# Optimization experiments

Hardware: AMD Instinct MI355X
Metric: run time of the kernel (lower is better)

Reference implementation:

```python
import jax, jax.numpy as jnp
import numpy as np

B, S, D, H, DK, DV = 4, 2048, 512, 8, 64, 64


def setup_inputs() -> dict:
    key0 = jax.random.key(0)
    ks = jax.random.split(key0, 11)
    w = 0.02
    return {
        "query": jax.random.normal(ks[0], (B, S, D), dtype=jnp.float32),
        "key": jax.random.normal(ks[1], (B, S, D), dtype=jnp.float32),
        "value": jax.random.normal(ks[2], (B, S, D), dtype=jnp.float32),
        "Wq": jax.random.normal(ks[3], (D, DK), dtype=jnp.float32) * w,
        "bq": jnp.zeros((DK,), dtype=jnp.float32),
        "Wk": jax.random.normal(ks[4], (D, DK), dtype=jnp.float32) * w,
        "bk": jnp.zeros((DK,), dtype=jnp.float32),
        "Wv": jax.random.normal(ks[5], (D, DV), dtype=jnp.float32) * w,
        "bv": jnp.zeros((DV,), dtype=jnp.float32),
        "Wo": jax.random.normal(ks[6], (H * DV, D), dtype=jnp.float32) * w,
        "bo": jnp.zeros((D,), dtype=jnp.float32),
    }


def reference(query, key, value, Wq, bq, Wk, bk, Wv, bv, Wo, bo):
    # NOTE: original module applies the SAME Dense layers to every head
    # (q_list = [self.query(query) for _ in range(heads)]), so all H heads
    # are mathematically identical -> compute one head and replicate.
    # NOTE: V is projected from `key`, not `value` (faithful to source bug).
    q = query @ Wq + bq          # [B, S, DK]
    k = key @ Wk + bk            # [B, S, DK]
    v = key @ Wv + bv            # [B, S, DV]
    scale = np.sqrt(DK).astype(np.float32)
    scores = jnp.einsum("bqd,bkd->bqk", q, k) / scale  # [B, S, S]
    # masked_mha=True and training=True -> causal mask, fill -1e19
    causal = jnp.triu(jnp.ones((S, S), dtype=scores.dtype), 1)
    scores = scores + causal * jnp.asarray(-1e19, scores.dtype)
    attn = jax.nn.softmax(scores, axis=-1)              # [B, S, S]
    o = jnp.einsum("bqk,bkv->bqv", attn, v)             # [B, S, DV]
    # concat of H identical heads along last axis == tile
    concat = jnp.tile(o, (1, 1, H))                     # [B, S, H*DV]
    return concat @ Wo + bo                             # [B, S, D]
```

## Files before the change

kernel.cpp:

```cpp
#include <hip/hip_runtime.h>
#include <hip/hip_bf16.h>


#define BB 4
#define SS 2048
#define BS (BB*SS)
#define MSHIFT 8.0f

typedef __bf16 v8bf __attribute__((ext_vector_type(8)));
typedef __bf16 v4bf __attribute__((ext_vector_type(4)));
typedef float  v4f  __attribute__((ext_vector_type(4)));

__device__ inline v8bf cvt8(float4 f0, float4 f1) {
    v8bf r;
    r[0] = (__bf16)f0.x; r[1] = (__bf16)f0.y; r[2] = (__bf16)f0.z; r[3] = (__bf16)f0.w;
    r[4] = (__bf16)f1.x; r[5] = (__bf16)f1.y; r[6] = (__bf16)f1.z; r[7] = (__bf16)f1.w;
    return r;
}

__global__ __launch_bounds__(256) void projprep_kernel(
    const float* __restrict__ query, const float* __restrict__ key,
    const float* __restrict__ Wq, const float* __restrict__ bq,
    const float* __restrict__ Wk, const float* __restrict__ bk,
    const float* __restrict__ Wv, const float* __restrict__ bv,
    const float* __restrict__ Wo,
    __bf16* __restrict__ Qp, __bf16* __restrict__ Kp, __bf16* __restrict__ Vt,
    __bf16* __restrict__ WoEt)
{
    __shared__ __bf16 Ws[2][16][520];
    const int t  = threadIdx.x;
    const int vb = blockIdx.x;

    if (vb >= 1024) {
        const int k = vb - 1024;
        for (int d = t; d < 512; d += 256) {
            float sum = 0.f;
#pragma unroll
            for (int h = 0; h < 8; h++) sum += Wo[(size_t)(h * 64 + k) * 512 + d];
            WoEt[d * 64 + k] = (__bf16)sum;
        }
        return;
    }

    const int lane = t & 63, w = t >> 6, lq = lane & 15, quad = lane >> 4;
    const int kind = vb >> 9;
    const int v2   = vb & 511;
    const int cb   = (v2 & 3) * 16;
    const int rows = (v2 >> 2) * 64 + w * 16;
    const float qscale = 0.125f * 1.44269504088896340736f;

    {
        const int c4 = (t & 3) * 4;
        const int kk = t >> 2;
        if (kind == 0) {
#pragma unroll
            for (int pass = 0; pass < 8; pass++) {
                int k = kk + pass * 64;
                float4 f = *(const float4*)(Wq + (size_t)k * 64 + cb + c4);
                Ws[0][c4 + 0][k] = (__bf16)(f.x * qscale);
                Ws[0][c4 + 1][k] = (__bf16)(f.y * qscale);
                Ws[0][c4 + 2][k] = (__bf16)(f.z * qscale);
                Ws[0][c4 + 3][k] = (__bf16)(f.w * qscale);
            }
        } else {
#pragma unroll
            for (int pass = 0; pass < 8; pass++) {
                int k = kk + pass * 64;
                float4 fk = *(const float4*)(Wk + (size_t)k * 64 + cb + c4);
                float4 fv = *(const float4*)(Wv + (size_t)k * 64 + cb + c4);
                Ws[0][c4 + 0][k] = (__bf16)fk.x;
                Ws[0][c4 + 1][k] = (__bf16)fk.y;
                Ws[0][c4 + 2][k] = (__bf16)fk.z;
                Ws[0][c4 + 3][k] = (__bf16)fk.w;
                Ws[1][c4 + 0][k] = (__bf16)fv.x;
                Ws[1][c4 + 1][k] = (__bf16)fv.y;
                Ws[1][c4 + 2][k] = (__bf16)fv.z;
                Ws[1][c4 + 3][k] = (__bf16)fv.w;
            }
        }
    }
    __syncthreads();

    const float* arow = ((kind == 0) ? query : key) + (size_t)(rows + lq) * 512;

    if (kind == 0) {
        const float bb = bq[cb + lq] * qscale;
        v4f acc = {bb, bb, bb, bb};
#pragma unroll 4
        for (int k0 = 0; k0 < 512; k0 += 32) {
            float4 f0 = *(const float4*)(arow + k0 + quad * 8);
            float4 f1 = *(const float4*)(arow + k0 + quad * 8 + 4);
            v8bf a = cvt8(f0, f1);
            v8bf b = *(const v8bf*)&Ws[0][lq][k0 + quad * 8];
            acc = __builtin_amdgcn_mfma_f32_16x16x32_bf16(a, b, acc, 0, 0, 0);
        }
#pragma unroll
        for (int r = 0; r < 4; r++)
            Qp[(size_t)(rows + quad * 4 + r) * 64 + cb + lq] = (__bf16)acc[r];
    } else {
        const float bk_ = bk[cb + lq], bv_ = bv[cb + lq];
        v4f ak = {bk_, bk_, bk_, bk_}, av = {bv_, bv_, bv_, bv_};
#pragma unroll 4
        for (int k0 = 0; k0 < 512; k0 += 32) {
            float4 f0 = *(const float4*)(arow + k0 + quad * 8);
            float4 f1 = *(const float4*)(arow + k0 + quad * 8 + 4);
            v8bf a  = cvt8(f0, f1);
            v8bf b0 = *(const v8bf*)&Ws[0][lq][k0 + quad * 8];
            v8bf b1 = *(const v8bf*)&Ws[1][lq][k0 + quad * 8];
            ak = __builtin_amdgcn_mfma_f32_16x16x32_bf16(a, b0, ak, 0, 0, 0);
            av = __builtin_amdgcn_mfma_f32_16x16x32_bf16(a, b1, av, 0, 0, 0);
        }
#pragma unroll
        for (int r = 0; r < 4; r++)
            Kp[(size_t)(rows + quad * 4 + r) * 64 + cb + lq] = (__bf16)ak[r];
        v4bf o4; o4[0] = (__bf16)av[0]; o4[1] = (__bf16)av[1];
        o4[2] = (__bf16)av[2]; o4[3] = (__bf16)av[3];
        *(v4bf*)&Vt[(size_t)(cb + lq) * BS + rows + quad * 4] = o4;
    }
}

__global__ __launch_bounds__(512) void attn_kernel(
    const __bf16* __restrict__ Qp,
    const __bf16* __restrict__ Kp,
    const __bf16* __restrict__ Vt,
    const __bf16* __restrict__ WoEt,
    const float* __restrict__ bo,
    float* __restrict__ out)
{
    __shared__ __bf16 Ks[64][72];
    __shared__ __bf16 Vs[64][72];
    __shared__ __bf16 Ps[8][16][72];

    const int t    = threadIdx.x;
    const int lane = t & 63;
    const int w8   = t >> 6;
    const int wv   = w8 & 3;
    const int b    = blockIdx.x & 3;
    const int jp   = blockIdx.x >> 2;
    const int qt   = jp * 2 + (w8 >> 2);
    const int qbase = qt * 64;
    const int Lmax = (jp + 1) * 128;
    const size_t bbase = (size_t)b * SS;

    const int lq   = lane & 15;
    const int quad = lane >> 4;
    const int qrow_w = qbase + wv * 16;
    const int wmax   = qrow_w + 15;

    const size_t qoff = (bbase + qrow_w + lq) * 64;
    v8bf qa0 = *(const v8bf*)(Qp + qoff + quad * 8);
    v8bf qa1 = *(const v8bf*)(Qp + qoff + 32 + quad * 8);

    v8bf ones;
#pragma unroll
    for (int i = 0; i < 8; i++) ones[i] = (__bf16)1.0f;

    v4f o[4] = {};
    v4f lacc = {};

    const int ky = t >> 3, dd = (t & 7) * 8;

    v8bf kpre = *(const v8bf*)(Kp + (bbase + ky) * 64 + dd);
    v8bf vpre = *(const v8bf*)(Vt + (size_t)ky * BS + bbase + dd);

    for (int kb = 0; kb < Lmax; kb += 64) {
        __syncthreads();
        *(v8bf*)&Ks[ky][dd] = kpre;
        *(v8bf*)&Vs[ky][dd] = vpre;
        if (kb + 64 < Lmax) {
            kpre = *(const v8bf*)(Kp + (bbase + kb + 64 + ky) * 64 + dd);
            vpre = *(const v8bf*)(Vt + (size_t)ky * BS + bbase + kb + 64 + dd);
        }
        __syncthreads();
        if (kb > wmax) continue;

        v4f s[4];
#pragma unroll
        for (int n = 0; n < 4; n++) {
            v8bf ka  = *(const v8bf*)&Ks[n * 16 + lq][quad * 8];
            v8bf kb2 = *(const v8bf*)&Ks[n * 16 + lq][32 + quad * 8];
            v4f z = {0.f, 0.f, 0.f, 0.f};
            z    = __builtin_amdgcn_mfma_f32_16x16x32_bf16(qa0, ka,  z, 0, 0, 0);
            s[n] = __builtin_amdgcn_mfma_f32_16x16x32_bf16(qa1, kb2, z, 0, 0, 0);
        }

        const int row0 = qrow_w + quad * 4;
        const int col0 = kb + lq;
#pragma unroll
        for (int n = 0; n < 4; n++)
#pragma unroll
            for (int r = 0; r < 4; r++) {
                float e = exp2f(s[n][r] - MSHIFT);
                e = (col0 + n * 16 > row0 + r) ? 0.f : e;
                Ps[w8][quad * 4 + r][n * 16 + lq] = (__bf16)e;
            }
        v8bf pa0 = *(const v8bf*)&Ps[w8][lq][quad * 8];
        v8bf pa1 = *(const v8bf*)&Ps[w8][lq][32 + quad * 8];

        lacc = __builtin_amdgcn_mfma_f32_16x16x32_bf16(pa0, ones, lacc, 0, 0, 0);
        lacc = __builtin_amdgcn_mfma_f32_16x16x32_bf16(pa1, ones, lacc, 0, 0, 0);

#pragma unroll
        for (int vt2 = 0; vt2 < 4; vt2++) {
            v8bf vb0 = *(const v8bf*)&Vs[vt2 * 16 + lq][quad * 8];
            v8bf vb1 = *(const v8bf*)&Vs[vt2 * 16 + lq][32 + quad * 8];
            o[vt2] = __builtin_amdgcn_mfma_f32_16x16x32_bf16(pa0, vb0, o[vt2], 0, 0, 0);
            o[vt2] = __builtin_amdgcn_mfma_f32_16x16x32_bf16(pa1, vb1, o[vt2], 0, 0, 0);
        }
    }

    __syncthreads();
    __bf16 (*Os)[72] = (w8 >> 2) ? Vs : Ks;
#pragma unroll
    for (int r = 0; r < 4; r++) {
        const float inv = 1.f / lacc[r];
#pragma unroll
        for (int vt2 = 0; vt2 < 4; vt2++)
            Os[wv * 16 + quad * 4 + r][vt2 * 16 + lq] = (__bf16)(o[vt2][r] * inv);
    }
    __syncthreads();

    {
        v8bf a0 = *(const v8bf*)&Os[wv * 16 + lq][quad * 8];
        v8bf a1 = *(const v8bf*)&Os[wv * 16 + lq][32 + quad * 8];
        const size_t orow = bbase + qbase + wv * 16;
#pragma unroll 4
        for (int i = 0; i < 32; i++) {
            const int cb2 = i * 16;
            v8bf b0 = *(const v8bf*)(WoEt + (size_t)(cb2 + lq) * 64 + quad * 8);
            v8bf b1 = *(const v8bf*)(WoEt + (size_t)(cb2 + lq) * 64 + 32 + quad * 8);
            const float bb2 = bo[cb2 + lq];
            v4f acc = {bb2, bb2, bb2, bb2};
            acc = __builtin_amdgcn_mfma_f32_16x16x32_bf16(a0, b0, acc, 0, 0, 0);
            acc = __builtin_amdgcn_mfma_f32_16x16x32_bf16(a1, b1, acc, 0, 0, 0);
#pragma unroll
            for (int r = 0; r < 4; r++)
                out[(orow + quad * 4 + r) * 512 + cb2 + lq] = acc[r];
        }
    }
}

extern "C" void kernel_launch(void* const* d_in, const int* in_sizes, int n_in,
                              void* d_out, int out_size, void* d_ws, size_t ws_size,
                              hipStream_t stream) {
    const float* query = (const float*)d_in[0];
    const float* key   = (const float*)d_in[1];
    const float* Wq = (const float*)d_in[3];
    const float* bq = (const float*)d_in[4];
    const float* Wk = (const float*)d_in[5];
    const float* bk = (const float*)d_in[6];
    const float* Wv = (const float*)d_in[7];
    const float* bv = (const float*)d_in[8];
    const float* Wo = (const float*)d_in[9];
    const float* bo = (const float*)d_in[10];
    float* out = (float*)d_out;

    char* p = (char*)d_ws;
    __bf16* Qp   = (__bf16*)p; p += (size_t)BS * 64 * 2;
    __bf16* Kp   = (__bf16*)p; p += (size_t)BS * 64 * 2;
    __bf16* Vtg  = (__bf16*)p; p += (size_t)BS * 64 * 2;
    __bf16* WoEt = (__bf16*)p; p += (size_t)64 * 512 * 2;

    projprep_kernel<<<1088, 256, 0, stream>>>(
        query, key, Wq, bq, Wk, bk, Wv, bv, Wo, Qp, Kp, Vtg, WoEt);
    attn_kernel<<<64, 512, 0, stream>>>(Qp, Kp, Vtg, WoEt, bo, out);
}
```

Baseline: 177.5 us.

## Split KV range across two wave groups per query tile, merge partials

Each block now handles a single 64-row query tile instead of two. Its two 4-wave groups process alternating 64-key blocks of a 128-key staged tile, and their partial O and row-sum accumulators are merged through shared memory. The output projection columns are also split between the groups. This doubles the grid from 64 to 128 blocks to fill more CUs, at the cost of larger LDS tiles, an extra merge and sync, and some idle waves on the diagonal tile.

```diff
diff --git a/kernel.cpp b/kernel.cpp
--- a/kernel.cpp
+++ b/kernel.cpp
@@ -127,19 +127,19 @@
     const float* __restrict__ bo,
     float* __restrict__ out)
 {
-    __shared__ __bf16 Ks[64][72];
-    __shared__ __bf16 Vs[64][72];
+    __shared__ __bf16 Ks[128][72];
+    __shared__ __bf16 Vs[64][136];
     __shared__ __bf16 Ps[8][16][72];
 
     const int t    = threadIdx.x;
     const int lane = t & 63;
     const int w8   = t >> 6;
     const int wv   = w8 & 3;
+    const int grp  = w8 >> 2;
     const int b    = blockIdx.x & 3;
-    const int jp   = blockIdx.x >> 2;
-    const int qt   = jp * 2 + (w8 >> 2);
+    const int qt   = blockIdx.x >> 2;
     const int qbase = qt * 64;
-    const int Lmax = (jp + 1) * 128;
+    const int L    = qbase + 64;
     const size_t bbase = (size_t)b * SS;
 
     const int lq   = lane & 15;
@@ -158,65 +158,91 @@
     v4f o[4] = {};
     v4f lacc = {};
 
-    const int ky = t >> 3, dd = (t & 7) * 8;
-
-    v8bf kpre = *(const v8bf*)(Kp + (bbase + ky) * 64 + dd);
-    v8bf vpre = *(const v8bf*)(Vt + (size_t)ky * BS + bbase + dd);
-
-    for (int kb = 0; kb < Lmax; kb += 64) {
+    const int ky = t >> 3;
+    const int dd = (t & 7) * 8;
+
+    v8bf kp0 = *(const v8bf*)(Kp + (bbase + ky) * 64 + dd);
+    v8bf kp1 = *(const v8bf*)(Kp + (bbase + 64 + ky) * 64 + dd);
+    v8bf vp0 = *(const v8bf*)(Vt + (size_t)ky * BS + bbase + dd);
+    v8bf vp1 = *(const v8bf*)(Vt + (size_t)ky * BS + bbase + 64 + dd);
+
+    for (int kb0 = 0; kb0 < L; kb0 += 128) {
         __syncthreads();
-        *(v8bf*)&Ks[ky][dd] = kpre;
-        *(v8bf*)&Vs[ky][dd] = vpre;
-        if (kb + 64 < Lmax) {
-            kpre = *(const v8bf*)(Kp + (bbase + kb + 64 + ky) * 64 + dd);
-            vpre = *(const v8bf*)(Vt + (size_t)ky * BS + bbase + kb + 64 + dd);
+        *(v8bf*)&Ks[ky][dd]       = kp0;
+        *(v8bf*)&Ks[ky + 64][dd]  = kp1;
+        *(v8bf*)&Vs[ky][dd]       = vp0;
+        *(v8bf*)&Vs[ky][64 + dd]  = vp1;
+        if (kb0 + 128 < L) {
+            kp0 = *(const v8bf*)(Kp + (bbase + kb0 + 128 + ky) * 64 + dd);
+            kp1 = *(const v8bf*)(Kp + (bbase + kb0 + 192 + ky) * 64 + dd);
+            vp0 = *(const v8bf*)(Vt + (size_t)ky * BS + bbase + kb0 + 128 + dd);
+            vp1 = *(const v8bf*)(Vt + (size_t)ky * BS + bbase + kb0 + 192 + dd);
         }
         __syncthreads();
-        if (kb > wmax) continue;
-
-        v4f s[4];
-#pragma unroll
-        for (int n = 0; n < 4; n++) {
-            v8bf ka  = *(const v8bf*)&Ks[n * 16 + lq][quad * 8];
-            v8bf kb2 = *(const v8bf*)&Ks[n * 16 + lq][32 + quad * 8];
-            v4f z = {0.f, 0.f, 0.f, 0.f};
-            z    = __builtin_amdgcn_mfma_f32_16x16x32_bf16(qa0, ka,  z, 0, 0, 0);
-            s[n] = __builtin_amdgcn_mfma_f32_16x16x32_bf16(qa1, kb2, z, 0, 0, 0);
-        }
-
-        const int row0 = qrow_w + quad * 4;
-        const int col0 = kb + lq;
-#pragma unroll
-        for (int n = 0; n < 4; n++)
-#pragma unroll
-            for (int r = 0; r < 4; r++) {
-                float e = exp2f(s[n][r] - MSHIFT);
-                e = (col0 + n * 16 > row0 + r) ? 0.f : e;
-                Ps[w8][quad * 4 + r][n * 16 + lq] = (__bf16)e;
-            }
-        v8bf pa0 = *(const v8bf*)&Ps[w8][lq][quad * 8];
-        v8bf pa1 = *(const v8bf*)&Ps[w8][lq][32 + quad * 8];
-
-        lacc = __builtin_amdgcn_mfma_f32_16x16x32_bf16(pa0, ones, lacc, 0, 0, 0);
-        lacc = __builtin_amdgcn_mfma_f32_16x16x32_bf16(pa1, ones, lacc, 0, 0, 0);
-
-#pragma unroll
-        for (int vt2 = 0; vt2 < 4; vt2++) {
-            v8bf vb0 = *(const v8bf*)&Vs[vt2 * 16 + lq][quad * 8];
-            v8bf vb1 = *(const v8bf*)&Vs[vt2 * 16 + lq][32 + quad * 8];
-            o[vt2] = __builtin_amdgcn_mfma_f32_16x16x32_bf16(pa0, vb0, o[vt2], 0, 0, 0);
-            o[vt2] = __builtin_amdgcn_mfma_f32_16x16x32_bf16(pa1, vb1, o[vt2], 0, 0, 0);
-        }
-    }
-
-    __syncthreads();
-    __bf16 (*Os)[72] = (w8 >> 2) ? Vs : Ks;
-#pragma unroll
-    for (int r = 0; r < 4; r++) {
-        const float inv = 1.f / lacc[r];
-#pragma unroll
-        for (int vt2 = 0; vt2 < 4; vt2++)
-            Os[wv * 16 + quad * 4 + r][vt2 * 16 + lq] = (__bf16)(o[vt2][r] * inv);
+
+        const int kb = kb0 + grp * 64;
+        if (kb <= wmax) {
+            v4f s[4];
+#pragma unroll
+            for (int n = 0; n < 4; n++) {
+                v8bf ka  = *(const v8bf*)&Ks[grp * 64 + n * 16 + lq][quad * 8];
+                v8bf kb2 = *(const v8bf*)&Ks[grp * 64 + n * 16 + lq][32 + quad * 8];
+                v4f z = {0.f, 0.f, 0.f, 0.f};
+                z    = __builtin_amdgcn_mfma_f32_16x16x32_bf16(qa0, ka,  z, 0, 0, 0);
+                s[n] = __builtin_amdgcn_mfma_f32_16x16x32_bf16(qa1, kb2, z, 0, 0, 0);
+            }
+
+            const int row0 = qrow_w + quad * 4;
+            const int col0 = kb + lq;
+#pragma unroll
+            for (int n = 0; n < 4; n++)
+#pragma unroll
+                for (int r = 0; r < 4; r++) {
+                    float e = exp2f(s[n][r] - MSHIFT);
+                    e = (col0 + n * 16 > row0 + r) ? 0.f : e;
+                    Ps[w8][quad * 4 + r][n * 16 + lq] = (__bf16)e;
+                }
+            v8bf pa0 = *(const v8bf*)&Ps[w8][lq][quad * 8];
+            v8bf pa1 = *(const v8bf*)&Ps[w8][lq][32 + quad * 8];
+
+            lacc = __builtin_amdgcn_mfma_f32_16x16x32_bf16(pa0, ones, lacc, 0, 0, 0);
+            lacc = __builtin_amdgcn_mfma_f32_16x16x32_bf16(pa1, ones, lacc, 0, 0, 0);
+
+#pragma unroll
+            for (int vt2 = 0; vt2 < 4; vt2++) {
+                v8bf vb0 = *(const v8bf*)&Vs[vt2 * 16 + lq][grp * 64 + quad * 8];
+                v8bf vb1 = *(const v8bf*)&Vs[vt2 * 16 + lq][grp * 64 + 32 + quad * 8];
+                o[vt2] = __builtin_amdgcn_mfma_f32_16x16x32_bf16(pa0, vb0, o[vt2], 0, 0, 0);
+                o[vt2] = __builtin_amdgcn_mfma_f32_16x16x32_bf16(pa1, vb1, o[vt2], 0, 0, 0);
+            }
+        }
+    }
+
+    __syncthreads();
+    float* Om = (float*)&Ks[0][0];
+    float* Lm = (float*)&Ps[0][0][0];
+    if (grp == 1) {
+#pragma unroll
+        for (int r = 0; r < 4; r++) {
+#pragma unroll
+            for (int vt2 = 0; vt2 < 4; vt2++)
+                Om[(wv * 16 + quad * 4 + r) * 64 + vt2 * 16 + lq] = o[vt2][r];
+        }
+        if (lq < 4) Lm[wv * 16 + quad * 4 + lq] = lacc[lq];
+    }
+    __syncthreads();
+    __bf16 (*Os)[136] = Vs;
+    if (grp == 0) {
+#pragma unroll
+        for (int r = 0; r < 4; r++) {
+            const int row = wv * 16 + quad * 4 + r;
+            const float inv = 1.f / (lacc[r] + Lm[row]);
+#pragma unroll
+            for (int vt2 = 0; vt2 < 4; vt2++) {
+                float val = o[vt2][r] + Om[row * 64 + vt2 * 16 + lq];
+                Os[row][vt2 * 16 + lq] = (__bf16)(val * inv);
+            }
+        }
     }
     __syncthreads();
 
@@ -225,8 +251,8 @@
         v8bf a1 = *(const v8bf*)&Os[wv * 16 + lq][32 + quad * 8];
         const size_t orow = bbase + qbase + wv * 16;
 #pragma unroll 4
-        for (int i = 0; i < 32; i++) {
-            const int cb2 = i * 16;
+        for (int i = 0; i < 16; i++) {
+            const int cb2 = (grp * 16 + i) * 16;
             v8bf b0 = *(const v8bf*)(WoEt + (size_t)(cb2 + lq) * 64 + quad * 8);
             v8bf b1 = *(const v8bf*)(WoEt + (size_t)(cb2 + lq) * 64 + 32 + quad * 8);
             const float bb2 = bo[cb2 + lq];
@@ -263,5 +289,5 @@
 
     projprep_kernel<<<1088, 256, 0, stream>>>(
         query, key, Wq, bq, Wk, bk, Wv, bv, Wo, Qp, Kp, Vtg, WoEt);
-    attn_kernel<<<64, 512, 0, stream>>>(Qp, Kp, Vtg, WoEt, bo, out);
-}
+    attn_kernel<<<128, 512, 0, stream>>>(Qp, Kp, Vtg, WoEt, bo, out);
+}
```

After: 153.6 us. -13.5%, faster.
